# Optimization experiments

Measured on AMD Instinct MI355X. Metric: run time of the kernel, lower is better.

The kernel has to match this reference:

```python
import jax, jax.numpy as jnp
import numpy as np

N = 100_000   # nodes
E = 1_600_000 # edges
F = 128       # feature_dim
H = 128       # hidden_dim
C = 16        # num_classes


def setup_inputs() -> dict:
    key = jax.random.key(0)
    ks = jax.random.split(key, 7)
    x = jax.random.normal(ks[0], (N, F), dtype=jnp.float32)
    edge_index = jax.random.randint(ks[1], (2, E), 0, N, dtype=jnp.int64)
    edge_attr = jax.random.uniform(ks[2], (E,), dtype=jnp.float32)
    W1 = jax.random.normal(ks[3], (F, H), dtype=jnp.float32) / np.float32(np.sqrt(F))
    b1 = jnp.zeros((H,), jnp.float32)
    W2 = jax.random.normal(ks[4], (H, C), dtype=jnp.float32) / np.float32(np.sqrt(H))
    b2 = jnp.zeros((C,), jnp.float32)
    return {"x": x, "edge_index": edge_index, "edge_attr": edge_attr,
            "W1": W1, "b1": b1, "W2": W2, "b2": b2}


def gcn_conv(x, src, dst, ew, W, b, n):
    # PyG GCNConv: add self-loops (weight 1), symmetric degree normalization,
    # linear transform, weighted scatter-sum to destinations, bias after aggregation.
    loop = jnp.arange(n, dtype=src.dtype)
    s = jnp.concatenate([src, loop])
    d = jnp.concatenate([dst, loop])
    w = jnp.concatenate([ew, jnp.ones((n,), ew.dtype)])
    deg = jax.ops.segment_sum(w, d, num_segments=n)           # [N]
    dinv = jnp.where(deg > 0, jax.lax.rsqrt(deg), 0.0)
    norm = dinv[s] * w * dinv[d]                               # [E+N]
    h = x @ W                                                  # [N, out]
    out = jax.ops.segment_sum(h[s] * norm[:, None], d, num_segments=n)
    return out + b


def reference(x, edge_index, edge_attr, W1, b1, W2, b2):
    src, dst = edge_index[0], edge_index[1]
    h = gcn_conv(x, src, dst, edge_attr, W1, b1, N)
    h = jax.nn.relu(h)
    # dropout is identity in eval mode
    h = gcn_conv(h, src, dst, edge_attr, W2, b2, N)
    return jax.nn.softmax(h, axis=1)
```

## Files before the change

kernel.cpp:

```cpp
#include <hip/hip_runtime.h>
#include <hip/hip_fp16.h>
#include <math.h>

#define SCAN_CHUNK 2048
#define NBLK 256
#define BSH 9
#define BNODES 512


typedef __attribute__((ext_vector_type(8))) _Float16 f16x8;
typedef __attribute__((ext_vector_type(16))) float f32x16;


__global__ __launch_bounds__(256) void k_prep(const float* __restrict__ W,
                                              __half* __restrict__ W1f) {
    int tid = blockIdx.x * 256 + threadIdx.x;
    if (tid < 16384) {
        int j  = tid & 7;
        int l  = (tid >> 3) & 63;
        int ks = (tid >> 9) & 7;
        int cb = tid >> 12;
        int c = cb * 32 + (l & 31);
        int k = (l >> 5) * 8 + ks * 16 + j;
        W1f[tid] = __float2half(W[(size_t)k * 128 + c]);
    }
}


__device__ __forceinline__ void gemm1_mfma(const float* __restrict__ x,
                                           const __half* __restrict__ W1f,
                                           __half* __restrict__ h1, int n,
                                           int row0, int t, char* smem) {
    __half (*xs)[136] = (__half (*)[136])smem;
#pragma unroll
    for (int it = 0; it < 4; ++it) {
        int idx = it * 256 + t;
        int r = idx >> 5, c4 = (idx & 31) * 4;
        int gr = row0 + r;
        float4 v = (gr < n) ? *(const float4*)(x + (size_t)gr * 128 + c4)
                            : make_float4(0.f, 0.f, 0.f, 0.f);
        union { __half2 h[2]; uint2 u; } pk;
        pk.h[0] = __floats2half2_rn(v.x, v.y);
        pk.h[1] = __floats2half2_rn(v.z, v.w);
        *(uint2*)&xs[r][c4] = pk.u;
    }
    __syncthreads();

    int wv = t >> 6, lane = t & 63;
    int m = lane & 31, kh = lane >> 5;
    int col0 = wv * 32;

    f16x8 a[8], b[8];
    const __half* bp = W1f + ((size_t)wv * 8 * 64 + lane) * 8;
#pragma unroll
    for (int ks = 0; ks < 8; ++ks)
        b[ks] = *(const f16x8*)(bp + (size_t)ks * 64 * 8);
#pragma unroll
    for (int ks = 0; ks < 8; ++ks)
        a[ks] = *(const f16x8*)&xs[m][kh * 8 + ks * 16];

    f32x16 acc;
#pragma unroll
    for (int r = 0; r < 16; ++r) acc[r] = 0.f;
#pragma unroll
    for (int ks = 0; ks < 8; ++ks)
        acc = __builtin_amdgcn_mfma_f32_32x32x16_f16(a[ks], b[ks], acc, 0, 0, 0);

#pragma unroll
    for (int r = 0; r < 16; ++r) {
        int row = (r & 3) + 8 * (r >> 2) + 4 * kh;
        int g = row0 + row;
        if (g < n) h1[(size_t)g * 128 + col0 + m] = __float2half(acc[r]);
    }
}

__device__ __forceinline__ long long sl_begin(int eb, int e) {
    return ((long long)eb * e / NBLK) & ~3LL;
}


__global__ __launch_bounds__(256) void kA(const int* __restrict__ dst, int e,
                                          int* __restrict__ hist, int nbuck,
                                          const float* __restrict__ x,
                                          const __half* __restrict__ W1f,
                                          __half* __restrict__ h1, int n,
                                          int nbB, int nbG, int gbase) {
    __shared__ char smem[32 * 136 * 2];
    int bid = blockIdx.x;
    long long T = nbB + nbG;
    long long g = ((long long)bid * nbG) / T;
    bool is_g = (((long long)(bid + 1) * nbG) / T) > g;
    int t = threadIdx.x;

    if (!is_g) {
        int* cnt = (int*)smem;
        int eb = bid - (int)g;
        for (int j = t; j < nbuck; j += 256) cnt[j] = 0;
        __syncthreads();
        long long e0 = sl_begin(eb, e);
        long long e1 = (eb == NBLK - 1) ? e : sl_begin(eb + 1, e);
        for (long long i = e0 + (long long)t * 4; i + 3 < e1; i += 1024) {
            int4 d4 = *(const int4*)(dst + i);
            atomicAdd(&cnt[d4.x >> BSH], 1);
            atomicAdd(&cnt[d4.y >> BSH], 1);
            atomicAdd(&cnt[d4.z >> BSH], 1);
            atomicAdd(&cnt[d4.w >> BSH], 1);
        }
        long long vend = e0 + ((e1 - e0) & ~3LL);
        for (long long i = vend + t; i < e1; i += 256)
            atomicAdd(&cnt[dst[i] >> BSH], 1);
        __syncthreads();
        for (int j = t; j < nbuck; j += 256)
            hist[(size_t)j * NBLK + eb] = cnt[j];
        return;
    }

    gemm1_mfma(x, W1f, h1, n, (gbase + (int)g) * 32, t, smem);
}


__global__ __launch_bounds__(256) void k_scanh(int* __restrict__ hist,
                                               int* __restrict__ bsum, int nh) {
    __shared__ int sh[256];
    int b = blockIdx.x, t = threadIdx.x;
    int base = b * SCAN_CHUNK + t * 8;
    int v[8];
    int s = 0;
#pragma unroll
    for (int j = 0; j < 8; ++j) {
        int i = base + j;
        v[j] = (i < nh) ? hist[i] : 0;
        s += v[j];
    }
    sh[t] = s;
    __syncthreads();
    for (int off = 1; off < 256; off <<= 1) {
        int u = (t >= off) ? sh[t - off] : 0;
        __syncthreads();
        sh[t] += u;
        __syncthreads();
    }
    int excl = (t > 0) ? sh[t - 1] : 0;
    if (t == 255) bsum[b] = sh[255];
    int run = excl;
#pragma unroll
    for (int j = 0; j < 8; ++j) {
        int i = base + j;
        if (i < nh) hist[i] = run;
        run += v[j];
    }
}

__device__ __forceinline__ void scan_bsum(const int* __restrict__ bsum, int nbS,
                                          int* boffs, int t) {
    if (t < 32) {
        int raw = (t < nbS) ? bsum[t] : 0;
        int v = raw;
        for (int off = 1; off < 32; off <<= 1) {
            int u = __shfl_up(v, off, 64);
            if (t >= off) v += u;
        }
        boffs[t] = v - raw;
    }
}


__global__ __launch_bounds__(256) void kB(const int* __restrict__ src,
                                          const int* __restrict__ dst,
                                          const float* __restrict__ ew, int e,
                                          const int* __restrict__ hist,
                                          const int* __restrict__ bsum, int nbS,
                                          int nbuck,
                                          int2* __restrict__ bucketed,
                                          const float* __restrict__ x,
                                          const __half* __restrict__ W1f,
                                          __half* __restrict__ h1, int n,
                                          int nbB, int nbG, int gbase) {
    __shared__ char smem[32 * 136 * 2];
    int bid = blockIdx.x;
    long long T = nbB + nbG;
    long long g = ((long long)bid * nbG) / T;
    bool is_g = (((long long)(bid + 1) * nbG) / T) > g;
    int t = threadIdx.x;

    if (!is_g) {
        int* wc = (int*)smem;
        int* boffs = (int*)(smem + 2048);
        int eb = bid - (int)g;
        scan_bsum(bsum, nbS, boffs, t);
        __syncthreads();
        for (int j = t; j < nbuck; j += 256) {
            int idx = j * NBLK + eb;
            wc[j] = hist[idx] + boffs[idx >> 11];
        }
        __syncthreads();
        long long e0 = sl_begin(eb, e);
        long long e1 = (eb == NBLK - 1) ? e : sl_begin(eb + 1, e);
        for (long long i = e0 + (long long)t * 4; i + 3 < e1; i += 1024) {
            int4 d4 = *(const int4*)(dst + i);
            int4 s4 = *(const int4*)(src + i);
            float4 w4 = *(const float4*)(ew + i);
            int2 rec;
            int pos;
            pos = atomicAdd(&wc[d4.x >> BSH], 1);
            rec.x = s4.x | ((d4.x & (BNODES - 1)) << 17);
            rec.y = __float_as_int(w4.x);
            bucketed[pos] = rec;
            pos = atomicAdd(&wc[d4.y >> BSH], 1);
            rec.x = s4.y | ((d4.y & (BNODES - 1)) << 17);
            rec.y = __float_as_int(w4.y);
            bucketed[pos] = rec;
            pos = atomicAdd(&wc[d4.z >> BSH], 1);
            rec.x = s4.z | ((d4.z & (BNODES - 1)) << 17);
            rec.y = __float_as_int(w4.z);
            bucketed[pos] = rec;
            pos = atomicAdd(&wc[d4.w >> BSH], 1);
            rec.x = s4.w | ((d4.w & (BNODES - 1)) << 17);
            rec.y = __float_as_int(w4.w);
            bucketed[pos] = rec;
        }
        long long vend = e0 + ((e1 - e0) & ~3LL);
        for (long long i = vend + t; i < e1; i += 256) {
            int d = dst[i];
            int b = d >> BSH;
            int pos = atomicAdd(&wc[b], 1);
            int2 rec;
            rec.x = src[i] | ((d & (BNODES - 1)) << 17);
            rec.y = __float_as_int(ew[i]);
            bucketed[pos] = rec;
        }
        return;
    }

    gemm1_mfma(x, W1f, h1, n, (gbase + (int)g) * 32, t, smem);
}


__global__ __launch_bounds__(256) void kC1(const int2* __restrict__ bucketed,
                                           const int* __restrict__ hist,
                                           const int* __restrict__ bsum, int nbS,
                                           int nbuck, int n, int e,
                                           int2* __restrict__ nodeinfo,
                                           const float* __restrict__ x,
                                           const __half* __restrict__ W1f,
                                           __half* __restrict__ h1, int gbase) {
    __shared__ char smem[32 * 136 * 2];
    int bid = blockIdx.x, t = threadIdx.x;

    if (bid >= nbuck) {
        gemm1_mfma(x, W1f, h1, n, (gbase + bid - nbuck) * 32, t, smem);
        return;
    }

    int*   cnts  = (int*)smem;
    float* degs  = (float*)(smem + 2048);
    int*   sh    = (int*)(smem + 4096);
    int*   boffs = (int*)(smem + 5120);
    int b = bid;

    scan_bsum(bsum, nbS, boffs, t);
    cnts[t] = 0; cnts[t + 256] = 0;
    degs[t] = 0.f; degs[t + 256] = 0.f;
    __syncthreads();

    int i0 = b * NBLK;
    int bstart = hist[i0] + boffs[i0 >> 11];
    int bend;
    if (b == nbuck - 1) bend = e;
    else {
        int i1 = (b + 1) * NBLK;
        bend = hist[i1] + boffs[i1 >> 11];
    }

    for (int i = bstart + t; i < bend; i += 256) {
        int2 rec = bucketed[i];
        int l = (rec.x >> 17) & (BNODES - 1);
        atomicAdd(&cnts[l], 1);
        atomicAdd(&degs[l], __int_as_float(rec.y));
    }
    __syncthreads();

    int c0 = cnts[2 * t], c1 = cnts[2 * t + 1];
    sh[t] = c0 + c1;
    __syncthreads();
    for (int off = 1; off < 256; off <<= 1) {
        int u = (t >= off) ? sh[t - off] : 0;
        __syncthreads();
        sh[t] += u;
        __syncthreads();
    }
    int excl = (t > 0) ? sh[t - 1] : 0;

    int rs0 = bstart + excl;
    int rs1 = rs0 + c0;
#pragma unroll
    for (int q = 0; q < 2; ++q) {
        int l = 2 * t + q;
        float dv = 1.0f / sqrtf(1.0f + degs[l]);
        int gnode = b * BNODES + l;
        if (gnode < n) {
            int2 ni;
            ni.x = (q == 0) ? rs0 : rs1;
            ni.y = __float_as_int(dv);
            nodeinfo[gnode] = ni;
        }
    }
    if (b == nbuck - 1 && t == 0) {
        int2 sent; sent.x = e; sent.y = 0;
        nodeinfo[n] = sent;
    }
}


__global__ __launch_bounds__(256) void kC2(const int2* __restrict__ bucketed,
                                           const int* __restrict__ hist,
                                           const int* __restrict__ bsum, int nbS,
                                           int nbuck, int n, int e,
                                           int2* __restrict__ csr,
                                           const int2* __restrict__ nodeinfo,
                                           const float* __restrict__ x,
                                           const __half* __restrict__ W1f,
                                           __half* __restrict__ h1, int gbase) {
    __shared__ char smem[32 * 136 * 2];
    int bid = blockIdx.x, t = threadIdx.x;

    if (bid >= nbuck) {
        gemm1_mfma(x, W1f, h1, n, (gbase + bid - nbuck) * 32, t, smem);
        return;
    }

    int* wcs   = (int*)smem;
    int* boffs = (int*)(smem + 2048);
    int b = bid;
    const int* nis = (const int*)nodeinfo;

    scan_bsum(bsum, nbS, boffs, t);
#pragma unroll
    for (int q = 0; q < 2; ++q) {
        int l = t + q * 256;
        int gnode = b * BNODES + l;
        wcs[l] = (gnode < n) ? nis[2 * (size_t)gnode] : 0;
    }
    __syncthreads();

    int i0 = b * NBLK;
    int bstart = hist[i0] + boffs[i0 >> 11];
    int bend;
    if (b == nbuck - 1) bend = e;
    else {
        int i1 = (b + 1) * NBLK;
        bend = hist[i1] + boffs[i1 >> 11];
    }

    for (int i = bstart + t; i < bend; i += 256) {
        int2 rec = bucketed[i];
        int l = (rec.x >> 17) & (BNODES - 1);
        int s = rec.x & 0x1FFFF;
        float dv = __int_as_float(nis[2 * (size_t)s + 1]);
        int pos = atomicAdd(&wcs[l], 1);
        int2 o;
        o.x = s;
        o.y = __float_as_int(__int_as_float(rec.y) * dv);
        csr[pos] = o;
    }
}


__global__ __launch_bounds__(256) void k_agg1(const __half* __restrict__ h1,
                                              const int2* __restrict__ nodeinfo,
                                              const int2* __restrict__ csr,
                                              const float* __restrict__ b1,
                                              const float* __restrict__ W2g,
                                              __half* __restrict__ h2, int n) {
    __shared__ float a1s[4][128];
    __shared__ float wt[16][132];
    int t = threadIdx.x;
#pragma unroll
    for (int it = 0; it < 8; ++it) {
        int idx = it * 256 + t;
        wt[idx & 15][idx >> 4] = W2g[idx];
    }
    int wv = t >> 6;
    int lane = t & 63;
    int grp = lane >> 4;
    int sl = lane & 15;
    int i = blockIdx.x * 4 + wv;
    float acc[8];
#pragma unroll
    for (int k = 0; k < 8; ++k) acc[k] = 0.f;
    float di = 0.f;
    if (i < n) {
        int2 ni = nodeinfo[i];
        int begin = ni.x;
        int end = ((const int*)nodeinfo)[(size_t)(i + 1) * 2];
        di = __int_as_float(ni.y);
        if (grp == 0) {
            uint4 sv = *((const uint4*)(h1 + (size_t)i * 128) + sl);
            const __half2* hp = (const __half2*)&sv;
#pragma unroll
            for (int k = 0; k < 4; ++k) {
                float2 f = __half22float2(hp[k]);
                acc[2 * k] = di * f.x; acc[2 * k + 1] = di * f.y;
            }
        }
        int len = end - begin;
        int m = (len + 3) >> 2;
        if (m > 0) {
            int j0 = begin + grp;
            bool v0 = j0 < end;
            int2 er0 = csr[v0 ? j0 : begin];
            float w0 = v0 ? __int_as_float(er0.y) : 0.f;
            uint4 hv0 = *((const uint4*)(h1 + (size_t)er0.x * 128) + sl);
            int j1 = j0 + 4;
            bool v1 = j1 < end;
            int2 er1 = csr[v1 ? j1 : begin];
            float w1 = v1 ? __int_as_float(er1.y) : 0.f;
            for (int it2 = 1; it2 < m; ++it2) {
                uint4 hv1 = *((const uint4*)(h1 + (size_t)er1.x * 128) + sl);
                int j2 = j1 + 4;
                bool v2 = j2 < end;
                int2 er2 = csr[v2 ? j2 : begin];
                float w2 = v2 ? __int_as_float(er2.y) : 0.f;
                const __half2* hp = (const __half2*)&hv0;
#pragma unroll
                for (int k = 0; k < 4; ++k) {
                    float2 f = __half22float2(hp[k]);
                    acc[2 * k]     += w0 * f.x;
                    acc[2 * k + 1] += w0 * f.y;
                }
                hv0 = hv1; w0 = w1;
                er1 = er2; w1 = w2; j1 = j2;
            }
            const __half2* hp = (const __half2*)&hv0;
#pragma unroll
            for (int k = 0; k < 4; ++k) {
                float2 f = __half22float2(hp[k]);
                acc[2 * k]     += w0 * f.x;
                acc[2 * k + 1] += w0 * f.y;
            }
        }
    }
#pragma unroll
    for (int k = 0; k < 8; ++k) {
        acc[k] += __shfl_xor(acc[k], 16, 64);
        acc[k] += __shfl_xor(acc[k], 32, 64);
    }
    if (i < n && grp == 0) {
#pragma unroll
        for (int k = 0; k < 8; ++k)
            a1s[wv][8 * sl + k] = fmaxf(di * acc[k] + b1[8 * sl + k], 0.f);
    }
    __syncthreads();
    int oi = t >> 2, q = t & 3;
    int node = oi >> 4, c = oi & 15;
    const float* arow = a1s[node];
    float accd = 0.f;
#pragma unroll
    for (int j = 0; j < 32; ++j) accd += arow[q + 4 * j] * wt[c][q + 4 * j];
    accd += __shfl_xor(accd, 1, 64);
    accd += __shfl_xor(accd, 2, 64);
    int gi = blockIdx.x * 4 + node;
    if (q == 0 && gi < n) h2[(size_t)gi * 16 + c] = __float2half(accd);
}


__global__ __launch_bounds__(256) void k_agg2(const __half* __restrict__ h2,
                                              const int2* __restrict__ nodeinfo,
                                              const int2* __restrict__ csr,
                                              const float* __restrict__ b2,
                                              float* __restrict__ out, int n) {
    int t = blockIdx.x * 256 + threadIdx.x;
    int i = t >> 4;
    int c = t & 15;
    if (i >= n) return;
    int2 ni = nodeinfo[i];
    int begin = ni.x;
    int end = ((const int*)nodeinfo)[(size_t)(i + 1) * 2];
    float di = __int_as_float(ni.y);
    float acc = di * __half2float(h2[(size_t)i * 16 + c]);
    int j = begin;
    for (; j + 4 <= end; j += 4) {
        int2 e0 = csr[j], e1 = csr[j + 1], e2 = csr[j + 2], e3 = csr[j + 3];
        float f0 = __half2float(h2[(size_t)e0.x * 16 + c]);
        float f1 = __half2float(h2[(size_t)e1.x * 16 + c]);
        float f2 = __half2float(h2[(size_t)e2.x * 16 + c]);
        float f3 = __half2float(h2[(size_t)e3.x * 16 + c]);
        acc += __int_as_float(e0.y) * f0;
        acc += __int_as_float(e1.y) * f1;
        acc += __int_as_float(e2.y) * f2;
        acc += __int_as_float(e3.y) * f3;
    }
    for (; j < end; ++j) {
        int2 e0 = csr[j];
        acc += __int_as_float(e0.y) * __half2float(h2[(size_t)e0.x * 16 + c]);
    }
    acc = di * acc + b2[c];
    float m = acc;
    for (int off = 8; off; off >>= 1) m = fmaxf(m, __shfl_xor(m, off, 16));
    float ex = expf(acc - m);
    float ssum = ex;
    for (int off = 8; off; off >>= 1) ssum += __shfl_xor(ssum, off, 16);
    out[(size_t)i * 16 + c] = ex / ssum;
}


extern "C" void kernel_launch(void* const* d_in, const int* in_sizes, int n_in,
                              void* d_out, int out_size, void* d_ws, size_t ws_size,
                              hipStream_t stream) {
    const float* x  = (const float*)d_in[0];
    const int*   ei = (const int*)d_in[1];
    const float* ew = (const float*)d_in[2];
    const float* W1 = (const float*)d_in[3];
    const float* b1 = (const float*)d_in[4];
    const float* W2 = (const float*)d_in[5];
    const float* b2 = (const float*)d_in[6];
    float* out = (float*)d_out;

    const int N = in_sizes[0] / 128;
    const int E = in_sizes[2];
    const int* src = ei;
    const int* dst = ei + E;

    const int nbuck = (N + BNODES - 1) >> BSH;
    const int nh = nbuck * NBLK;
    const int nbS = (nh + SCAN_CHUNK - 1) / SCAN_CHUNK;

    char* w = (char*)d_ws;
    int2*   bucketed = (int2*)w;              w += (size_t)E * 8;
    int2*   csr      = (int2*)w;              w += (size_t)E * 8;
    __half* h1       = (__half*)w;            w += (size_t)N * 128 * 2;
    __half* h2       = (__half*)w;            w += (size_t)N * 16 * 2;
    int2*   nodeinfo = (int2*)w;              w += (size_t)(N + 2) * 8;
    int*    hist     = (int*)w;               w += (size_t)nh * 4;
    int*    bsum     = (int*)w;               w += 64 * 4;
    __half* W1f      = (__half*)w;            w += (size_t)16384 * 2;

    int nbG_total = (N + 31) / 32;
    int nbG1 = 1250;
    int nbG2 = 1250;
    int nbG3 = 313;
    int nbG4 = nbG_total - nbG1 - nbG2 - nbG3;

    k_prep<<<64, 256, 0, stream>>>(W1, W1f);
    kA<<<NBLK + nbG1, 256, 0, stream>>>(dst, E, hist, nbuck, x, W1f, h1, N,
                                        NBLK, nbG1, 0);
    k_scanh<<<nbS, 256, 0, stream>>>(hist, bsum, nh);
    kB<<<NBLK + nbG2, 256, 0, stream>>>(src, dst, ew, E, hist, bsum, nbS, nbuck,
                                        bucketed, x, W1f, h1, N, NBLK, nbG2, nbG1);
    kC1<<<nbuck + nbG3, 256, 0, stream>>>(bucketed, hist, bsum, nbS, nbuck, N, E,
                                          nodeinfo, x, W1f, h1, nbG1 + nbG2);
    kC2<<<nbuck + nbG4, 256, 0, stream>>>(bucketed, hist, bsum, nbS, nbuck, N, E,
                                          csr, nodeinfo, x, W1f, h1,
                                          nbG1 + nbG2 + nbG3);
    k_agg1<<<(N + 3) / 4, 256, 0, stream>>>(h1, nodeinfo, csr, b1, W2, h2, N);
    k_agg2<<<(N + 15) / 16, 256, 0, stream>>>(h2, nodeinfo, csr, b2, out, N);
}
```

Before: 188.4 us.

## Pack count/degree atomics, vectorize agg2 to half2, rebalance GEMM block split

```diff
diff --git a/kernel.cpp b/kernel.cpp
--- a/kernel.cpp
+++ b/kernel.cpp
@@ -252,15 +252,13 @@
         return;
     }
 
-    int*   cnts  = (int*)smem;
-    float* degs  = (float*)(smem + 2048);
-    int*   sh    = (int*)(smem + 4096);
-    int*   boffs = (int*)(smem + 5120);
+    unsigned long long* cd = (unsigned long long*)smem;
+    int* sh    = (int*)(smem + 4096);
+    int* boffs = (int*)(smem + 5120);
     int b = bid;
 
     scan_bsum(bsum, nbS, boffs, t);
-    cnts[t] = 0; cnts[t + 256] = 0;
-    degs[t] = 0.f; degs[t + 256] = 0.f;
+    cd[t] = 0ULL; cd[t + 256] = 0ULL;
     __syncthreads();
 
     int i0 = b * NBLK;
@@ -275,12 +273,16 @@
     for (int i = bstart + t; i < bend; i += 256) {
         int2 rec = bucketed[i];
         int l = (rec.x >> 17) & (BNODES - 1);
-        atomicAdd(&cnts[l], 1);
-        atomicAdd(&degs[l], __int_as_float(rec.y));
-    }
-    __syncthreads();
-
-    int c0 = cnts[2 * t], c1 = cnts[2 * t + 1];
+        unsigned long long pk = (1ULL << 52) |
+            (unsigned long long)(long long)rintf(__int_as_float(rec.y) * 67108864.0f);
+        atomicAdd(&cd[l], pk);
+    }
+    __syncthreads();
+
+    unsigned long long v0 = cd[2 * t], v1 = cd[2 * t + 1];
+    int c0 = (int)(v0 >> 52), c1 = (int)(v1 >> 52);
+    float d0 = (float)(long long)(v0 & ((1ULL << 52) - 1)) * 1.4901161193847656e-8f;
+    float d1 = (float)(long long)(v1 & ((1ULL << 52) - 1)) * 1.4901161193847656e-8f;
     sh[t] = c0 + c1;
     __syncthreads();
     for (int off = 1; off < 256; off <<= 1) {
@@ -296,7 +298,7 @@
 #pragma unroll
     for (int q = 0; q < 2; ++q) {
         int l = 2 * t + q;
-        float dv = 1.0f / sqrtf(1.0f + degs[l]);
+        float dv = 1.0f / sqrtf(1.0f + ((q == 0) ? d0 : d1));
         int gnode = b * BNODES + l;
         if (gnode < n) {
             int2 ni;
@@ -470,37 +472,46 @@
                                               const float* __restrict__ b2,
                                               float* __restrict__ out, int n) {
     int t = blockIdx.x * 256 + threadIdx.x;
-    int i = t >> 4;
-    int c = t & 15;
+    int i = t >> 3;
+    int cp = t & 7;
     if (i >= n) return;
     int2 ni = nodeinfo[i];
     int begin = ni.x;
     int end = ((const int*)nodeinfo)[(size_t)(i + 1) * 2];
     float di = __int_as_float(ni.y);
-    float acc = di * __half2float(h2[(size_t)i * 16 + c]);
+    const __half2* h2p = (const __half2*)h2;
+    float2 self = __half22float2(h2p[(size_t)i * 8 + cp]);
+    float a0 = di * self.x, a1 = di * self.y;
     int j = begin;
     for (; j + 4 <= end; j += 4) {
         int2 e0 = csr[j], e1 = csr[j + 1], e2 = csr[j + 2], e3 = csr[j + 3];
-        float f0 = __half2float(h2[(size_t)e0.x * 16 + c]);
-        float f1 = __half2float(h2[(size_t)e1.x * 16 + c]);
-        float f2 = __half2float(h2[(size_t)e2.x * 16 + c]);
-        float f3 = __half2float(h2[(size_t)e3.x * 16 + c]);
-        acc += __int_as_float(e0.y) * f0;
-        acc += __int_as_float(e1.y) * f1;
-        acc += __int_as_float(e2.y) * f2;
-        acc += __int_as_float(e3.y) * f3;
+        float2 f0 = __half22float2(h2p[(size_t)e0.x * 8 + cp]);
+        float2 f1 = __half22float2(h2p[(size_t)e1.x * 8 + cp]);
+        float2 f2 = __half22float2(h2p[(size_t)e2.x * 8 + cp]);
+        float2 f3 = __half22float2(h2p[(size_t)e3.x * 8 + cp]);
+        float w0 = __int_as_float(e0.y), w1 = __int_as_float(e1.y);
+        float w2 = __int_as_float(e2.y), w3 = __int_as_float(e3.y);
+        a0 += w0 * f0.x; a1 += w0 * f0.y;
+        a0 += w1 * f1.x; a1 += w1 * f1.y;
+        a0 += w2 * f2.x; a1 += w2 * f2.y;
+        a0 += w3 * f3.x; a1 += w3 * f3.y;
     }
     for (; j < end; ++j) {
         int2 e0 = csr[j];
-        acc += __int_as_float(e0.y) * __half2float(h2[(size_t)e0.x * 16 + c]);
-    }
-    acc = di * acc + b2[c];
-    float m = acc;
-    for (int off = 8; off; off >>= 1) m = fmaxf(m, __shfl_xor(m, off, 16));
-    float ex = expf(acc - m);
-    float ssum = ex;
-    for (int off = 8; off; off >>= 1) ssum += __shfl_xor(ssum, off, 16);
-    out[(size_t)i * 16 + c] = ex / ssum;
+        float2 f0 = __half22float2(h2p[(size_t)e0.x * 8 + cp]);
+        float w0 = __int_as_float(e0.y);
+        a0 += w0 * f0.x; a1 += w0 * f0.y;
+    }
+    float2 bb = *(const float2*)(b2 + 2 * cp);
+    a0 = di * a0 + bb.x;
+    a1 = di * a1 + bb.y;
+    float m = fmaxf(a0, a1);
+    for (int off = 4; off; off >>= 1) m = fmaxf(m, __shfl_xor(m, off, 8));
+    float ex0 = expf(a0 - m), ex1 = expf(a1 - m);
+    float s = ex0 + ex1;
+    for (int off = 4; off; off >>= 1) s += __shfl_xor(s, off, 8);
+    float2 o; o.x = ex0 / s; o.y = ex1 / s;
+    *(float2*)(out + (size_t)i * 16 + 2 * cp) = o;
 }
 
 
@@ -536,9 +547,9 @@
     __half* W1f      = (__half*)w;            w += (size_t)16384 * 2;
 
     int nbG_total = (N + 31) / 32;
-    int nbG1 = 1250;
-    int nbG2 = 1250;
-    int nbG3 = 313;
+    int nbG1 = 1450;
+    int nbG2 = 1150;
+    int nbG3 = 275;
     int nbG4 = nbG_total - nbG1 - nbG2 - nbG3;
 
     k_prep<<<64, 256, 0, stream>>>(W1, W1f);
@@ -553,5 +564,5 @@
                                           csr, nodeinfo, x, W1f, h1,
                                           nbG1 + nbG2 + nbG3);
     k_agg1<<<(N + 3) / 4, 256, 0, stream>>>(h1, nodeinfo, csr, b1, W2, h2, N);
-    k_agg2<<<(N + 15) / 16, 256, 0, stream>>>(h2, nodeinfo, csr, b2, out, N);
-}
+    k_agg2<<<(N + 31) / 32, 256, 0, stream>>>(h2, nodeinfo, csr, b2, out, N);
+}
```

After: 178.7 us. 5.1% less time.
